# Performance work log

Hardware: AMD Instinct MI355X
Metric: run time of the kernel (lower is better)

The kernel has to match this reference:

```python
import jax, jax.numpy as jnp
import numpy as np

N, E, H, NH, S, EF, K = 25000, 400000, 64, 4, 16, 8, 2
HS = H // NH  # head size


def _ln(x, w, b):
    m = x.mean(-1, keepdims=True)
    v = ((x - m) ** 2).mean(-1, keepdims=True)
    return (x - m) / jnp.sqrt(v + 1e-5) * w + b


def _seg_softmax(scores, seg, n):
    # scores: [E, NH], seg: [E] -> softmax over edges sharing the same dest node
    mx = jax.ops.segment_max(scores, seg, num_segments=n)
    e = jnp.exp(scores - mx[seg])
    s = jax.ops.segment_sum(e, seg, num_segments=n)
    return e / (s[seg] + 1e-9)


def _edge_layer(h, x_s, src, dest, ef, w1, w2, proj, gated):
    # h: [N,H] (already layer-normed). Gather, fused per-edge MLP (no bias).
    inp = jnp.concatenate([h[src], h[dest], x_s[src], x_s[dest], ef], axis=-1)  # [E,168]
    raw = jnp.maximum(inp @ w1.T, 0.0) @ w2.T  # [E,NH]
    if gated:
        w = jax.nn.sigmoid(raw)
    else:
        w = _seg_softmax(jax.nn.leaky_relu(raw) / jnp.sqrt(jnp.asarray(HS, raw.dtype)), dest, N)
    msg = h.reshape(N, NH, HS)[src] * w[:, :, None]          # [E,NH,HS]
    agg = jax.ops.segment_sum(msg, dest, num_segments=N)     # [N,NH,HS]
    return agg.reshape(N, H) @ proj.T, w


def _mlp(x, w1, b1, w2, b2):
    return jnp.maximum(x @ w1.T + b1, 0.0) @ w2.T + b2


def _forward(x, x_s, edge_features, fwd_w1, fwd_w2, fwd_proj, rev_w1, rev_w2, rev_proj,
             ln_w, ln_b, r_w1, r_b1, r_w2, r_b2, z_w1, z_b1, z_w2, z_b2,
             c_w1, c_b1, c_w2, c_b2, edge_index):
    src, dest = edge_index[0], edge_index[1]
    # forward-direction stacked attention hops
    h_fwd, fwd_ws = x, []
    for k in range(K):
        h_norm = _ln(h_fwd, ln_w, ln_b)
        msg, w = _edge_layer(h_norm, x_s, src, dest, edge_features,
                             fwd_w1[k], fwd_w2[k], fwd_proj[k], gated=False)
        h_fwd = h_fwd + msg
        fwd_ws.append(w)
    fwd_ws = jnp.stack(fwd_ws, axis=-1)  # [E,NH,K]
    # reverse-direction stacked gating hops (edge direction flipped)
    h_rev, rev_ws = x, []
    for k in range(K):
        h_norm = _ln(h_rev, ln_w, ln_b)
        msg, w = _edge_layer(h_norm, x_s, dest, src, edge_features,
                             rev_w1[k], rev_w2[k], rev_proj[k], gated=True)
        h_rev = h_rev + msg
        rev_ws.append(w)
    rev_ws = jnp.stack(rev_ws, axis=-1)  # [E,NH,K]
    messages = jnp.concatenate([h_fwd - x, h_rev - x], axis=-1)  # [N,2H]
    gate_input = jnp.concatenate([x, messages], axis=-1)          # [N,3H]
    r_gate = jax.nn.sigmoid(_mlp(gate_input, r_w1, r_b1, r_w2, r_b2))
    z_gate = jax.nn.sigmoid(_mlp(gate_input, z_w1, z_b1, z_w2, z_b2))
    cand_in = jnp.concatenate([r_gate * x, messages], axis=-1)
    cand = jnp.tanh(_mlp(cand_in, c_w1, c_b1, c_w2, c_b2))
    final_h = (1.0 - z_gate) * x + z_gate * cand
    return final_h, fwd_ws, rev_ws, z_gate, r_gate


def setup_inputs() -> dict:
    key = jax.random.key(0)
    ks = jax.random.split(key, 20)
    mlp_in = 2 * H + 2 * S + EF  # 168
    width = 2 * H                # 128
    gi, gw = 3 * H, 3 * H        # 192, 192

    def nrm(k, shape, fan_in):
        return jax.random.normal(k, shape, jnp.float32) / np.sqrt(fan_in)

    return {
        'x': jax.random.normal(ks[0], (N, H), jnp.float32),
        'x_s': jax.random.normal(ks[1], (N, S), jnp.float32),
        'edge_index': jax.random.randint(ks[2], (2, E), 0, N, jnp.int32),
        'edge_features': jax.random.normal(ks[3], (E, EF), jnp.float32),
        'fwd_w1': nrm(ks[4], (K, width, mlp_in), mlp_in),
        'fwd_w2': nrm(ks[5], (K, NH, width), width),
        'fwd_proj': nrm(ks[6], (K, H, H), H),
        'rev_w1': nrm(ks[7], (K, width, mlp_in), mlp_in),
        'rev_w2': nrm(ks[8], (K, NH, width), width),
        'rev_proj': nrm(ks[9], (K, H, H), H),
        'ln_w': jnp.ones((H,), jnp.float32),
        'ln_b': jnp.zeros((H,), jnp.float32),
        'r_w1': nrm(ks[10], (gw, gi), gi), 'r_b1': jnp.zeros((gw,), jnp.float32),
        'r_w2': nrm(ks[11], (H, gw), gw), 'r_b2': jnp.zeros((H,), jnp.float32),
        'z_w1': nrm(ks[12], (gw, gi), gi), 'z_b1': jnp.zeros((gw,), jnp.float32),
        'z_w2': nrm(ks[13], (H, gw), gw), 'z_b2': jnp.zeros((H,), jnp.float32),
        'c_w1': nrm(ks[14], (gw, gi), gi), 'c_b1': jnp.zeros((gw,), jnp.float32),
        'c_w2': nrm(ks[15], (H, gw), gw), 'c_b2': jnp.zeros((H,), jnp.float32),
    }


def reference(x, x_s, edge_index, edge_features, fwd_w1, fwd_w2, fwd_proj,
              rev_w1, rev_w2, rev_proj, ln_w, ln_b, r_w1, r_b1, r_w2, r_b2,
              z_w1, z_b1, z_w2, z_b2, c_w1, c_b1, c_w2, c_b2):
    return _forward(x, x_s, edge_features, fwd_w1, fwd_w2, fwd_proj,
                    rev_w1, rev_w2, rev_proj, ln_w, ln_b,
                    r_w1, r_b1, r_w2, r_b2, z_w1, z_b1, z_w2, z_b2,
                    c_w1, c_b1, c_w2, c_b2, edge_index)
```

## Files before the change

### kernel.cpp

```cpp
#include <hip/hip_runtime.h>
#include <hip/hip_fp16.h>
#include <math.h>

#define NN 25000
#define EE 400000
#define HH 64
#define NHEAD 4
#define SDIM 16
#define EFDIM 8
#define KHOP 2
#define MIN 168
#define WID 128
#define GIN 192
#define KP 96

typedef __attribute__((ext_vector_type(8))) short bf16x8;
typedef __attribute__((ext_vector_type(4))) float f32x4;
typedef unsigned short ushortT;
typedef unsigned int uintT;

__device__ __forceinline__ float wave_sum64(float v) {
#pragma unroll
  for (int m = 1; m <= 32; m <<= 1) v += __shfl_xor(v, m, 64);
  return v;
}

__device__ __forceinline__ ushortT f2b(float f) {
  uintT u = __float_as_uint(f);
  return (ushortT)((u + 0x7FFFu + ((u >> 16) & 1u)) >> 16);
}
__device__ __forceinline__ float b2f(ushortT h) {
  return __uint_as_float(((uintT)h) << 16);
}

union U4H8 {
  uint4 u;
  __half2 h[4];
};

__device__ __forceinline__ __half2 relu2(__half2 v) {
  union { __half2 h; uintT u; } x;
  x.h = v;
  uintT mask = ((x.u & 0x80008000u) >> 15) * 0xFFFFu;
  x.u &= ~mask;
  return x.h;
}

__global__ void k_histo2(const int* __restrict__ src, const int* __restrict__ dst,
                         int* __restrict__ cnt_s, int* __restrict__ cnt_d) {
  int e = blockIdx.x * 256 + threadIdx.x;
  if (e < EE) {
    atomicAdd(&cnt_d[dst[e]], 1);
    atomicAdd(&cnt_s[src[e]], 1);
  }
}

__global__ void k_scan2(const int* __restrict__ cnt_d, const int* __restrict__ cnt_s,
                        int* __restrict__ rp_d, int* __restrict__ rp_s) {
  const int* cnt = blockIdx.x ? cnt_s : cnt_d;
  int* rp = blockIdx.x ? rp_s : rp_d;
  __shared__ int part[1024];
  int t = threadIdx.x;
  const int CH = (NN + 1023) / 1024;
  int base = t * CH;
  int s = 0;
  for (int i = 0; i < CH; ++i) {
    int j = base + i;
    if (j < NN) s += cnt[j];
  }
  part[t] = s;
  __syncthreads();
  for (int off = 1; off < 1024; off <<= 1) {
    int v = (t >= off) ? part[t - off] : 0;
    __syncthreads();
    part[t] += v;
    __syncthreads();
  }
  int run = (t == 0) ? 0 : part[t - 1];
  for (int i = 0; i < CH; ++i) {
    int j = base + i;
    if (j < NN) { rp[j] = run; run += cnt[j]; }
  }
  if (t == 1023) rp[NN] = run;
}

__global__ void k_scatter2(const int* __restrict__ src, const int* __restrict__ dst,
                           const int* __restrict__ rp_s, const int* __restrict__ rp_d,
                           int* __restrict__ cur_s, int* __restrict__ cur_d,
                           int* __restrict__ eid_s, int* __restrict__ eid_d) {
  int e = blockIdx.x * 256 + threadIdx.x;
  if (e < EE) {
    int nd = dst[e];
    int pd = atomicAdd(&cur_d[nd], 1);
    eid_d[rp_d[nd] + pd] = e;
    int ns = src[e];
    int ps = atomicAdd(&cur_s[ns], 1);
    eid_s[rp_s[ns] + ps] = e;
  }
}

__global__ __launch_bounds__(256) void k_sortseg2(const int* __restrict__ rp_d,
                                                  const int* __restrict__ rp_s,
                                                  int* __restrict__ eid_d,
                                                  int* __restrict__ eid_s) {
  int gw = blockIdx.x * 4 + (threadIdx.x >> 6);
  int lane = threadIdx.x & 63;
  if (gw >= 2 * NN) return;
  const int* rp = (gw < NN) ? rp_d : rp_s;
  int* eids = (gw < NN) ? eid_d : eid_s;
  int node = (gw < NN) ? gw : gw - NN;
  int beg = rp[node], end = rp[node + 1];
  int deg = end - beg;
  if (deg <= 1) return;
  if (deg <= 64) {
    int v = (lane < deg) ? eids[beg + lane] : 0x7fffffff;
#pragma unroll
    for (int k = 2; k <= 64; k <<= 1) {
#pragma unroll
      for (int j = k >> 1; j > 0; j >>= 1) {
        int other = __shfl_xor(v, j, 64);
        bool takeMin = (((lane & k) == 0) == ((lane & j) == 0));
        v = takeMin ? min(v, other) : max(v, other);
      }
    }
    if (lane < deg) eids[beg + lane] = v;
  } else if (lane == 0) {
    for (int i = beg + 1; i < end; ++i) {
      int v = eids[i];
      int j = i - 1;
      while (j >= beg && eids[j] > v) { eids[j + 1] = eids[j]; --j; }
      eids[j + 1] = v;
    }
  }
}

__global__ void k_mkpos2(const int* __restrict__ eid_d, const int* __restrict__ eid_s,
                         const int* __restrict__ src, const int* __restrict__ dst,
                         const float* __restrict__ ef, int4* __restrict__ pos_f,
                         int4* __restrict__ pos_r, uint4* __restrict__ efh_f,
                         uint4* __restrict__ efh_r) {
  int i = blockIdx.x * 256 + threadIdx.x;
  if (i >= EE) return;
  int e1 = eid_d[i];
  pos_f[i] = make_int4(e1, src[e1], dst[e1], 0);
  int e2 = eid_s[i];
  pos_r[i] = make_int4(e2, dst[e2], src[e2], 0);
  {
    float4 a0 = *(const float4*)(ef + (size_t)e1 * EFDIM);
    float4 a1 = *(const float4*)(ef + (size_t)e1 * EFDIM + 4);
    U4H8 u;
    u.h[0] = __floats2half2_rn(a0.x, a0.y);
    u.h[1] = __floats2half2_rn(a0.z, a0.w);
    u.h[2] = __floats2half2_rn(a1.x, a1.y);
    u.h[3] = __floats2half2_rn(a1.z, a1.w);
    efh_f[i] = u.u;
  }
  {
    float4 b0 = *(const float4*)(ef + (size_t)e2 * EFDIM);
    float4 b1 = *(const float4*)(ef + (size_t)e2 * EFDIM + 4);
    U4H8 u;
    u.h[0] = __floats2half2_rn(b0.x, b0.y);
    u.h[1] = __floats2half2_rn(b0.z, b0.w);
    u.h[2] = __floats2half2_rn(b1.x, b1.y);
    u.h[3] = __floats2half2_rn(b1.z, b1.w);
    efh_r[i] = u.u;
  }
}

#define PACKN (256 * KP + 512 + 256 + 4096)
__global__ void k_pack_bf(const float* __restrict__ fw1, const float* __restrict__ rw1,
                          const float* __restrict__ fw2, const float* __restrict__ rw2,
                          const float* __restrict__ fpj, const float* __restrict__ rpj,
                          ushortT* __restrict__ pAB_all, __half2* __restrict__ w1e2_all,
                          __half2* __restrict__ w22_all, ushortT* __restrict__ pj_all) {
  int y = blockIdx.y;
  const float* w1 = (y < 2) ? fw1 + (size_t)y * WID * MIN
                            : rw1 + (size_t)(y - 2) * WID * MIN;
  const float* w2 = (y < 2) ? fw2 + (size_t)y * NHEAD * WID
                            : rw2 + (size_t)(y - 2) * NHEAD * WID;
  const float* pj = (y < 2) ? fpj + (size_t)y * HH * HH
                            : rpj + (size_t)(y - 2) * HH * HH;
  int i = blockIdx.x * 256 + threadIdx.x;
  if (i < 256 * KP) {
    int j = i / KP, k = i % KP;
    float v = 0.f;
    if (k < 80) {
      int row = (j < 128) ? j : j - 128;
      int col = (j < 128) ? (k < 64 ? k : k + 64) : (k < 64 ? k + 64 : k + 80);
      v = w1[row * MIN + col];
    }
    pAB_all[(size_t)y * 256 * KP + i] = f2b(v);
  } else if (i < 256 * KP + 512) {
    int jj = i - 256 * KP;
    int f = jj >> 6, jp = jj & 63;
    w1e2_all[y * 512 + jj] =
        __floats2half2_rn(w1[(2 * jp) * MIN + 160 + f], w1[(2 * jp + 1) * MIN + 160 + f]);
  } else if (i < 256 * KP + 512 + 256) {
    int jj = i - 256 * KP - 512;
    int o = jj >> 6, jp = jj & 63;
    w22_all[y * 256 + jj] = __floats2half2_rn(w2[o * WID + 2 * jp], w2[o * WID + 2 * jp + 1]);
  } else if (i < PACKN) {
    int jj = i - 256 * KP - 512 - 256;
    pj_all[y * 4096 + jj] = f2b(pj[jj]);
  }
}

#define CW1 (GIN * GIN)
#define CW2 (HH * GIN)
__global__ void k_cvt6(const float* __restrict__ r_w1, const float* __restrict__ z_w1,
                       const float* __restrict__ c_w1, const float* __restrict__ r_w2,
                       const float* __restrict__ z_w2, const float* __restrict__ c_w2,
                       ushortT* __restrict__ rzw1, ushortT* __restrict__ cw1,
                       ushortT* __restrict__ rw2, ushortT* __restrict__ zw2,
                       ushortT* __restrict__ cw2) {
  int i = blockIdx.x * 256 + threadIdx.x;
  if (i < CW1) rzw1[i] = f2b(r_w1[i]);
  else if (i < 2 * CW1) rzw1[i] = f2b(z_w1[i - CW1]);
  else if (i < 3 * CW1) cw1[i - 2 * CW1] = f2b(c_w1[i - 2 * CW1]);
  else if (i < 3 * CW1 + CW2) rw2[i - 3 * CW1] = f2b(r_w2[i - 3 * CW1]);
  else if (i < 3 * CW1 + 2 * CW2) zw2[i - 3 * CW1 - CW2] = f2b(z_w2[i - 3 * CW1 - CW2]);
  else if (i < 3 * CW1 + 3 * CW2) cw2[i - 3 * CW1 - 2 * CW2] = f2b(c_w2[i - 3 * CW1 - 2 * CW2]);
}

__global__ __launch_bounds__(256) void k_ln_init(
    const float* __restrict__ x, const float* __restrict__ xs,
    const float* __restrict__ lw, const float* __restrict__ lb,
    ushortT* __restrict__ ncf0, ushortT* __restrict__ ncr0,
    ushortT* __restrict__ ncf1, ushortT* __restrict__ ncr1) {
  int t = threadIdx.x;
  int node = blockIdx.x * 4 + (t >> 6), lane = t & 63;
  if (node >= NN) return;
  float v = x[(size_t)node * HH + lane];
  float mean = wave_sum64(v) * (1.0f / 64.0f);
  float d = v - mean;
  float var = wave_sum64(d * d) * (1.0f / 64.0f);
  ushortT val = f2b(d * rsqrtf(var + 1e-5f) * lw[lane] + lb[lane]);
  ncf0[(size_t)node * KP + lane] = val;
  ncr0[(size_t)node * KP + lane] = val;
  if (lane < SDIM) {
    ushortT xv = f2b(xs[(size_t)node * SDIM + lane]);
    ncf0[(size_t)node * KP + HH + lane] = xv;
    ncr0[(size_t)node * KP + HH + lane] = xv;
    ncf1[(size_t)node * KP + HH + lane] = xv;
    ncr1[(size_t)node * KP + HH + lane] = xv;
    ncf0[(size_t)node * KP + 80 + lane] = 0;
    ncr0[(size_t)node * KP + 80 + lane] = 0;
    ncf1[(size_t)node * KP + 80 + lane] = 0;
    ncr1[(size_t)node * KP + 80 + lane] = 0;
  }
}

__global__ __launch_bounds__(256) void k_proj2(
    const ushortT* __restrict__ Af, const ushortT* __restrict__ Ar,
    const ushortT* __restrict__ Wf, const ushortT* __restrict__ Wr,
    ushortT* __restrict__ Cf, ushortT* __restrict__ Cr) {
  const ushortT* A = blockIdx.y ? Ar : Af;
  const ushortT* W = blockIdx.y ? Wr : Wf;
  ushortT* C = blockIdx.y ? Cr : Cf;
  int w = threadIdx.x >> 6, l = threadIdx.x & 63;
  int m0 = blockIdx.x * 64 + w * 16;
  int rowa = m0 + (l & 15);
  int kb = l >> 4;
  bf16x8 afr0 = {0,0,0,0,0,0,0,0}, afr1 = afr0, afr2 = afr0;
  if (rowa < NN) {
    const ushortT* ap = A + (size_t)rowa * KP + kb * 8;
    afr0 = *(const bf16x8*)(ap);
    afr1 = *(const bf16x8*)(ap + 32);
    afr2 = *(const bf16x8*)(ap + 64);
  }
  int crow = m0 + (l >> 4) * 4;
  int ccol0 = l & 15;
  for (int n0 = 0; n0 < 256; n0 += 64) {
    f32x4 acc[4];
#pragma unroll
    for (int n = 0; n < 4; ++n) acc[n] = (f32x4){0.f, 0.f, 0.f, 0.f};
    const ushortT* wbase = W + (size_t)(n0 + (l & 15)) * KP + kb * 8;
#pragma unroll
    for (int n = 0; n < 4; ++n) {
      const ushortT* wp = wbase + (size_t)(16 * n) * KP;
      acc[n] = __builtin_amdgcn_mfma_f32_16x16x32_bf16(afr0, *(const bf16x8*)(wp), acc[n], 0, 0, 0);
      acc[n] = __builtin_amdgcn_mfma_f32_16x16x32_bf16(afr1, *(const bf16x8*)(wp + 32), acc[n], 0, 0, 0);
      acc[n] = __builtin_amdgcn_mfma_f32_16x16x32_bf16(afr2, *(const bf16x8*)(wp + 64), acc[n], 0, 0, 0);
    }
#pragma unroll
    for (int n = 0; n < 4; ++n) {
      int col = n0 + ccol0 + n * 16;
#pragma unroll
      for (int r = 0; r < 4; ++r) {
        int row = crow + r;
        if (row < NN)
          C[(size_t)row * 256 + col] = __half_as_ushort(__float2half(acc[n][r]));
      }
    }
  }
}

template <int ACT, int BF16OUT, int KD>
__global__ __launch_bounds__(256) void k_gemm2(
    const ushortT* __restrict__ A, int lda, const ushortT* __restrict__ W,
    const float* __restrict__ bias, void* __restrict__ Cout, int ldc, int M, int Nc,
    const float* __restrict__ zv, const float* __restrict__ xp) {
  constexpr int KS = KD / 32;
  int w = threadIdx.x >> 6, l = threadIdx.x & 63;
  int m0 = blockIdx.x * 64 + w * 16;
  int rowa = m0 + (l & 15);
  int kb = l >> 4;
  bf16x8 afr[KS];
#pragma unroll
  for (int ks = 0; ks < KS; ++ks) {
    afr[ks] = (bf16x8){0, 0, 0, 0, 0, 0, 0, 0};
    if (rowa < M) afr[ks] = *(const bf16x8*)(A + (size_t)rowa * lda + ks * 32 + kb * 8);
  }
  int crow = m0 + (l >> 4) * 4;
  int ccol0 = l & 15;
  for (int n0 = 0; n0 < Nc; n0 += 64) {
    f32x4 acc[4];
#pragma unroll
    for (int n = 0; n < 4; ++n) acc[n] = (f32x4){0.f, 0.f, 0.f, 0.f};
    const ushortT* wbase = W + (size_t)(n0 + (l & 15)) * KD + kb * 8;
#pragma unroll
    for (int n = 0; n < 4; ++n) {
      const ushortT* wp = wbase + (size_t)(16 * n) * KD;
#pragma unroll
      for (int ks = 0; ks < KS; ++ks)
        acc[n] = __builtin_amdgcn_mfma_f32_16x16x32_bf16(afr[ks], *(const bf16x8*)(wp + ks * 32),
                                                         acc[n], 0, 0, 0);
    }
#pragma unroll
    for (int n = 0; n < 4; ++n) {
      int col = n0 + ccol0 + n * 16;
      float bv = bias ? bias[col] : 0.f;
#pragma unroll
      for (int r = 0; r < 4; ++r) {
        int row = crow + r;
        if (row < M) {
          float v = acc[n][r] + bv;
          if (ACT == 1) v = fmaxf(v, 0.f);
          else if (ACT == 2) v = 1.f / (1.f + expf(-v));
          else if (ACT == 3) v = tanhf(v);
          else if (ACT == 5) {
            float z = zv[(size_t)row * HH + col];
            float xv = xp[(size_t)row * HH + col];
            v = (1.f - z) * xv + z * tanhf(v);
          }
          if (BF16OUT)
            ((ushortT*)Cout)[(size_t)row * ldc + col] = f2b(v);
          else
            ((float*)Cout)[(size_t)row * ldc + col] = v;
        }
      }
    }
  }
}

__global__ __launch_bounds__(256) void k_gemm_rz(
    const ushortT* __restrict__ hid, const ushortT* __restrict__ rw2,
    const ushortT* __restrict__ zw2, const float* __restrict__ rb2,
    const float* __restrict__ zb2, float* __restrict__ outR, float* __restrict__ outZ,
    const float* __restrict__ x, ushortT* __restrict__ gi) {
  int y = blockIdx.y;
  const ushortT* A = hid + (y ? GIN : 0);
  const ushortT* W = y ? zw2 : rw2;
  const float* bias = y ? zb2 : rb2;
  float* C = y ? outZ : outR;
  constexpr int KS = GIN / 32;
  int w = threadIdx.x >> 6, l = threadIdx.x & 63;
  int m0 = blockIdx.x * 64 + w * 16;
  int rowa = m0 + (l & 15);
  int kb = l >> 4;
  bf16x8 afr[KS];
#pragma unroll
  for (int ks = 0; ks < KS; ++ks) {
    afr[ks] = (bf16x8){0, 0, 0, 0, 0, 0, 0, 0};
    if (rowa < NN) afr[ks] = *(const bf16x8*)(A + (size_t)rowa * 384 + ks * 32 + kb * 8);
  }
  int crow = m0 + (l >> 4) * 4;
  int ccol0 = l & 15;
  f32x4 acc[4];
#pragma unroll
  for (int n = 0; n < 4; ++n) acc[n] = (f32x4){0.f, 0.f, 0.f, 0.f};
  const ushortT* wbase = W + (size_t)(l & 15) * GIN + kb * 8;
#pragma unroll
  for (int n = 0; n < 4; ++n) {
    const ushortT* wp = wbase + (size_t)(16 * n) * GIN;
#pragma unroll
    for (int ks = 0; ks < KS; ++ks)
      acc[n] = __builtin_amdgcn_mfma_f32_16x16x32_bf16(afr[ks], *(const bf16x8*)(wp + ks * 32),
                                                       acc[n], 0, 0, 0);
  }
#pragma unroll
  for (int n = 0; n < 4; ++n) {
    int col = ccol0 + n * 16;
    float bv = bias[col];
#pragma unroll
    for (int r = 0; r < 4; ++r) {
      int row = crow + r;
      if (row < NN) {
        float v = acc[n][r] + bv;
        float sig = 1.f / (1.f + expf(-v));
        C[(size_t)row * HH + col] = sig;
        if (y == 0)
          gi[(size_t)row * GIN + col] = f2b(sig * x[(size_t)row * HH + col]);
      }
    }
  }
}

__global__ __launch_bounds__(256) void k_edge3(
    const ushortT* __restrict__ cABf, const ushortT* __restrict__ cABr,
    const int4* __restrict__ pos_f, const int4* __restrict__ pos_r,
    const uint4* __restrict__ efh_f, const uint4* __restrict__ efh_r,
    const __half2* __restrict__ w1e2_f, const __half2* __restrict__ w1e2_r,
    const __half2* __restrict__ w22_f, const __half2* __restrict__ w22_r,
    float* __restrict__ s_seq, float* __restrict__ outRW,
    float* __restrict__ ws_seq, int hop) {
  int y = blockIdx.y;
  const __half2* cAB2 = (const __half2*)(y ? cABr : cABf);
  const int4* pos = y ? pos_r : pos_f;
  const uint4* efh = y ? efh_r : efh_f;
  const __half2* w1e2 = y ? w1e2_r : w1e2_f;
  const __half2* w22 = y ? w22_r : w22_f;
  __shared__ __half2 w1e2_s[8][64];
  __shared__ __half2 w22_s[4][64];
  int t = threadIdx.x;
  for (int i = t; i < 512; i += 256) w1e2_s[i >> 6][i & 63] = w1e2[i];
  if (t < 256) w22_s[t >> 6][t & 63] = w22[t];
  __syncthreads();
  int es = t >> 2, q = t & 3;
  size_t ii = (size_t)blockIdx.x * 64 + es;
  int4 pr = pos[ii];
  const __half2* cA2 = cAB2 + (size_t)pr.y * 128;
  const __half2* cB2 = cAB2 + (size_t)pr.z * 128 + 64;
  U4H8 efu;
  efu.u = efh[ii];
  __half2 efb[8];
#pragma unroll
  for (int f2v = 0; f2v < 4; ++f2v) {
    efb[2 * f2v] = __half2half2(__low2half(efu.h[f2v]));
    efb[2 * f2v + 1] = __half2half2(__high2half(efu.h[f2v]));
  }
  float pf[4] = {0.f, 0.f, 0.f, 0.f};
#pragma unroll
  for (int c = 0; c < 4; ++c) {
    int jp0 = c * 16 + q * 4;
    U4H8 ua, ub;
    ua.u = *(const uint4*)(cA2 + jp0);
    ub.u = *(const uint4*)(cB2 + jp0);
    __half2 h2v[4];
#pragma unroll
    for (int i2 = 0; i2 < 4; ++i2) h2v[i2] = __hadd2(ua.h[i2], ub.h[i2]);
#pragma unroll
    for (int f = 0; f < 8; ++f) {
      U4H8 wv;
      wv.u = *(const uint4*)(&w1e2_s[f][jp0]);
#pragma unroll
      for (int i2 = 0; i2 < 4; ++i2) h2v[i2] = __hfma2(efb[f], wv.h[i2], h2v[i2]);
    }
#pragma unroll
    for (int i2 = 0; i2 < 4; ++i2) h2v[i2] = relu2(h2v[i2]);
#pragma unroll
    for (int o = 0; o < 4; ++o) {
      U4H8 wv;
      wv.u = *(const uint4*)(&w22_s[o][jp0]);
      __half2 p2 = __hmul2(h2v[0], wv.h[0]);
      p2 = __hfma2(h2v[1], wv.h[1], p2);
      p2 = __hfma2(h2v[2], wv.h[2], p2);
      p2 = __hfma2(h2v[3], wv.h[3], p2);
      pf[o] += __low2float(p2) + __high2float(p2);
    }
  }
#pragma unroll
  for (int m = 1; m <= 2; m <<= 1) {
    pf[0] += __shfl_xor(pf[0], m, 64);
    pf[1] += __shfl_xor(pf[1], m, 64);
    pf[2] += __shfl_xor(pf[2], m, 64);
    pf[3] += __shfl_xor(pf[3], m, 64);
  }
  float pv = (q == 0) ? pf[0] : (q == 1) ? pf[1] : (q == 2) ? pf[2] : pf[3];
  if (y) {
    float sig = 1.f / (1.f + expf(-pv));
    outRW[(size_t)pr.x * (NHEAD * KHOP) + q * KHOP + hop] = sig;
    ws_seq[ii * 4 + q] = sig;
  } else {
    s_seq[ii * 4 + q] = (pv > 0.f ? pv : 0.01f * pv) * 0.25f;
  }
}

__global__ __launch_bounds__(256) void k_softagg5(
    const ushortT* __restrict__ ncf, const ushortT* __restrict__ ncr,
    const float* __restrict__ s_seq, const float* __restrict__ ws_seq, int hop,
    const int* __restrict__ rp_d, const int* __restrict__ rp_s,
    const int4* __restrict__ pos_f, const int4* __restrict__ pos_r,
    ushortT* __restrict__ agg_f, ushortT* __restrict__ agg_r,
    float* __restrict__ wout) {
  int y = blockIdx.y;
  const ushortT* hn_bf = y ? ncr : ncf;
  const int* rp = y ? rp_s : rp_d;
  const int4* pos = y ? pos_r : pos_f;
  ushortT* agg = y ? agg_r : agg_f;
  __shared__ float w_s[4][64][4];
  __shared__ int ot_s[4][64];
  int t = threadIdx.x;
  int wvi = t >> 6, lane = t & 63;
  int node = blockIdx.x * 4 + wvi;
  if (node >= NN) return;
  int beg = rp[node], end = rp[node + 1];
  int deg = end - beg;
  bool small = (deg <= 64);
  float mxv = 0.f, invv = 0.f;
  int li = lane >> 2, o = lane & 3;
  if (deg > 0 && small) {
    int i0 = beg + li;
    if (y == 0) {
      int ee4[4];
      float sv[4];
#pragma unroll
      for (int u = 0; u < 4; ++u) {
        int idx = i0 + u * 16;
        bool val = idx < end;
        int4 pr = pos[val ? idx : beg];
        ee4[u] = pr.x;
        if (o == 0 && val) ot_s[wvi][li + u * 16] = pr.y * KP;
        float v = s_seq[(size_t)(val ? idx : beg) * 4 + o];
        sv[u] = val ? v : -1e30f;
      }
      float mx = fmaxf(fmaxf(sv[0], sv[1]), fmaxf(sv[2], sv[3]));
#pragma unroll
      for (int m = 4; m <= 32; m <<= 1) mx = fmaxf(mx, __shfl_xor(mx, m, 64));
      float ex[4];
      float sum = 0.f;
#pragma unroll
      for (int u = 0; u < 4; ++u) {
        ex[u] = (sv[u] > -1e29f) ? expf(sv[u] - mx) : 0.f;
        sum += ex[u];
      }
#pragma unroll
      for (int m = 4; m <= 32; m <<= 1) sum += __shfl_xor(sum, m, 64);
      float inv = 1.f / (sum + 1e-9f);
#pragma unroll
      for (int u = 0; u < 4; ++u) {
        if (i0 + u * 16 < end) {
          float wv = ex[u] * inv;
          wout[(size_t)ee4[u] * (NHEAD * KHOP) + o * KHOP + hop] = wv;
          w_s[wvi][li + u * 16][o] = wv;
        }
      }
    } else {
#pragma unroll
      for (int u = 0; u < 4; ++u) {
        int idx = i0 + u * 16;
        bool val = idx < end;
        if (val) {
          if (o == 0) {
            int4 pr = pos[idx];
            ot_s[wvi][li + u * 16] = pr.y * KP;
          }
          w_s[wvi][li + u * 16][o] = ws_seq[(size_t)idx * 4 + o];
        }
      }
    }
  } else if (deg > 0) {
    if (y == 0) {
      float mx = -1e30f;
      for (int ii = beg + li; ii < end; ii += 16)
        mx = fmaxf(mx, s_seq[(size_t)ii * 4 + o]);
#pragma unroll
      for (int m = 4; m <= 32; m <<= 1) mx = fmaxf(mx, __shfl_xor(mx, m, 64));
      float sum = 0.f;
      for (int ii = beg + li; ii < end; ii += 16)
        sum += expf(s_seq[(size_t)ii * 4 + o] - mx);
#pragma unroll
      for (int m = 4; m <= 32; m <<= 1) sum += __shfl_xor(sum, m, 64);
      float inv = 1.f / (sum + 1e-9f);
      for (int ii = beg + li; ii < end; ii += 16) {
        wout[(size_t)pos[ii].x * (NHEAD * KHOP) + o * KHOP + hop] =
            expf(s_seq[(size_t)ii * 4 + o] - mx) * inv;
      }
      mxv = mx;
      invv = inv;
    }
  }
  int hd = lane >> 4;
  float acc = 0.f;
  if (small) {
    for (int ii = 0; ii < deg; ii += 8) {
#pragma unroll
      for (int u = 0; u < 8; ++u) {
        int ed = ii + u;
        int edc = (ed < deg) ? ed : 0;
        int ot = ot_s[wvi][edc];
        float w = w_s[wvi][edc][hd];
        float hv = b2f(hn_bf[(size_t)ot + lane]);
        acc += ((ed < deg) ? w : 0.f) * hv;
      }
    }
  } else {
    float mx_hd = 0.f, inv_hd = 0.f;
    if (y == 0) {
      mx_hd = __shfl(mxv, hd, 64);
      inv_hd = __shfl(invv, hd, 64);
    }
    for (int ii = beg; ii < end; ++ii) {
      int4 pr = pos[ii];
      float w;
      if (y == 0)
        w = expf(s_seq[(size_t)ii * 4 + hd] - mx_hd) * inv_hd;
      else
        w = ws_seq[(size_t)ii * 4 + hd];
      acc += w * b2f(hn_bf[(size_t)pr.y * KP + lane]);
    }
  }
  agg[(size_t)node * HH + lane] = f2b(acc);
}

template <int DO_LN, int DO_GATE>
__global__ __launch_bounds__(256) void k_projout(
    const ushortT* __restrict__ agg_f, const ushortT* __restrict__ agg_r,
    const ushortT* __restrict__ pj_f, const ushortT* __restrict__ pj_r,
    float* __restrict__ h_f, float* __restrict__ h_r,
    ushortT* __restrict__ ncf_n, ushortT* __restrict__ ncr_n,
    const float* __restrict__ lnw, const float* __restrict__ lnb,
    const float* __restrict__ x, ushortT* __restrict__ gi) {
  int y = blockIdx.y;
  const ushortT* A = y ? agg_r : agg_f;
  const ushortT* W = y ? pj_r : pj_f;
  float* h = y ? h_r : h_f;
  ushortT* ncat_n = y ? ncr_n : ncf_n;
  int w = threadIdx.x >> 6, l = threadIdx.x & 63;
  int m0 = blockIdx.x * 64 + w * 16;
  int rowa = m0 + (l & 15);
  int kb = l >> 4;
  bf16x8 afr0 = {0, 0, 0, 0, 0, 0, 0, 0}, afr1 = afr0;
  if (rowa < NN) {
    afr0 = *(const bf16x8*)(A + (size_t)rowa * HH + kb * 8);
    afr1 = *(const bf16x8*)(A + (size_t)rowa * HH + 32 + kb * 8);
  }
  f32x4 acc[4];
#pragma unroll
  for (int n = 0; n < 4; ++n) acc[n] = (f32x4){0.f, 0.f, 0.f, 0.f};
  const ushortT* wbase = W + (size_t)(l & 15) * HH + kb * 8;
#pragma unroll
  for (int n = 0; n < 4; ++n) {
    const ushortT* wp = wbase + (size_t)(16 * n) * HH;
    acc[n] = __builtin_amdgcn_mfma_f32_16x16x32_bf16(afr0, *(const bf16x8*)(wp), acc[n], 0, 0, 0);
    acc[n] = __builtin_amdgcn_mfma_f32_16x16x32_bf16(afr1, *(const bf16x8*)(wp + 32), acc[n], 0, 0, 0);
  }
  int crow = m0 + (l >> 4) * 4;
  int ccol0 = l & 15;
#pragma unroll
  for (int r = 0; r < 4; ++r) {
    int row = crow + r;
    if (row >= NN) continue;
    float hv[4];
#pragma unroll
    for (int n = 0; n < 4; ++n)
      hv[n] = h[(size_t)row * HH + ccol0 + n * 16] + acc[n][r];
    float s = hv[0] + hv[1] + hv[2] + hv[3];
#pragma unroll
    for (int m = 1; m <= 8; m <<= 1) s += __shfl_xor(s, m, 64);
    float mean = s * (1.0f / 64.0f);
    float ss = 0.f;
#pragma unroll
    for (int n = 0; n < 4; ++n) {
      float d = hv[n] - mean;
      ss += d * d;
    }
#pragma unroll
    for (int m = 1; m <= 8; m <<= 1) ss += __shfl_xor(ss, m, 64);
    float rstd = rsqrtf(ss * (1.0f / 64.0f) + 1e-5f);
#pragma unroll
    for (int n = 0; n < 4; ++n) {
      int col = ccol0 + n * 16;
      size_t g = (size_t)row * HH + col;
      h[g] = hv[n];
      if (DO_LN)
        ncat_n[(size_t)row * KP + col] = f2b((hv[n] - mean) * rstd * lnw[col] + lnb[col]);
      if (DO_GATE) {
        float xv = x[g];
        if (y == 0) {
          gi[(size_t)row * GIN + col] = f2b(xv);
          gi[(size_t)row * GIN + 64 + col] = f2b(hv[n] - xv);
        } else {
          gi[(size_t)row * GIN + 128 + col] = f2b(hv[n] - xv);
        }
      }
    }
  }
}

extern "C" void kernel_launch(void* const* d_in, const int* in_sizes, int n_in,
                              void* d_out, int out_size, void* d_ws, size_t ws_size,
                              hipStream_t stream) {
  const float* x = (const float*)d_in[0];
  const float* xs = (const float*)d_in[1];
  const int* ei = (const int*)d_in[2];
  const float* ef = (const float*)d_in[3];
  const float* fw1 = (const float*)d_in[4];
  const float* fw2 = (const float*)d_in[5];
  const float* fpj = (const float*)d_in[6];
  const float* rw1 = (const float*)d_in[7];
  const float* rw2 = (const float*)d_in[8];
  const float* rpj = (const float*)d_in[9];
  const float* lnw = (const float*)d_in[10];
  const float* lnb = (const float*)d_in[11];
  const float* r_w1 = (const float*)d_in[12];
  const float* r_b1 = (const float*)d_in[13];
  const float* r_w2 = (const float*)d_in[14];
  const float* r_b2 = (const float*)d_in[15];
  const float* z_w1 = (const float*)d_in[16];
  const float* z_b1 = (const float*)d_in[17];
  const float* z_w2 = (const float*)d_in[18];
  const float* z_b2 = (const float*)d_in[19];
  const float* c_w1 = (const float*)d_in[20];
  const float* c_b1 = (const float*)d_in[21];
  const float* c_w2 = (const float*)d_in[22];
  const float* c_b2 = (const float*)d_in[23];
  const int* srcp = ei;
  const int* dstp = ei + EE;

  float* outF = (float*)d_out;
  float* outFW = outF + (size_t)NN * HH;
  float* outRW = outFW + (size_t)EE * NHEAD * KHOP;
  float* outZ = outRW + (size_t)EE * NHEAD * KHOP;
  float* outR = outZ + (size_t)NN * HH;

  char* Wb = (char*)d_ws;
  size_t off = 0;
  auto alloc = [&](size_t bytes) -> void* {
    void* p = Wb + off;
    off += (bytes + 255) & ~(size_t)255;
    return p;
  };
  float* h_fwd = (float*)alloc((size_t)NN * HH * 4);
  float* h_rev = (float*)alloc((size_t)NN * HH * 4);
  ushortT* ncat_f0 = (ushortT*)alloc((size_t)NN * KP * 2);
  ushortT* ncat_r0 = (ushortT*)alloc((size_t)NN * KP * 2);
  ushortT* ncat_f1 = (ushortT*)alloc((size_t)NN * KP * 2);
  ushortT* ncat_r1 = (ushortT*)alloc((size_t)NN * KP * 2);
  float* s_seq = (float*)alloc((size_t)EE * NHEAD * 4);
  float* ws_seq = (float*)alloc((size_t)EE * NHEAD * 4);
  char* big = (char*)alloc((size_t)2 * NN * 256 * 2);
  ushortT* cAB_f = (ushortT*)big;
  ushortT* cAB_r = (ushortT*)(big + (size_t)NN * 256 * 2);
  ushortT* hid_bf = (ushortT*)big;
  ushortT* gi_bf = (ushortT*)alloc((size_t)NN * GIN * 2);
  ushortT* agg_f = (ushortT*)alloc((size_t)NN * HH * 2);
  ushortT* agg_r = (ushortT*)alloc((size_t)NN * HH * 2);
  ushortT* packAB_bf = (ushortT*)alloc((size_t)4 * 256 * KP * 2);
  __half2* w1e2h = (__half2*)alloc((size_t)4 * 512 * 4);
  __half2* w22h = (__half2*)alloc((size_t)4 * 256 * 4);
  ushortT* pj_bf = (ushortT*)alloc((size_t)4 * 4096 * 2);
  ushortT* rzw1_bf = (ushortT*)alloc((size_t)384 * GIN * 2);
  ushortT* rw2_bf = (ushortT*)alloc((size_t)HH * GIN * 2);
  ushortT* zw2_bf = (ushortT*)alloc((size_t)HH * GIN * 2);
  ushortT* cw1_bf = (ushortT*)alloc((size_t)GIN * GIN * 2);
  ushortT* cw2_bf = (ushortT*)alloc((size_t)HH * GIN * 2);
  float* rz_b1 = (float*)alloc(384 * 4);
  int* rp_d = (int*)alloc((NN + 8) * 4);
  int* rp_s = (int*)alloc((NN + 8) * 4);
  int* cur2 = (int*)alloc((size_t)2 * NN * 4);
  int* cur_d = cur2;
  int* cur_s = cur2 + NN;
  int* eid_d = (int*)alloc((size_t)EE * 4);
  int* eid_s = (int*)alloc((size_t)EE * 4);
  int4* pos_f = (int4*)alloc((size_t)EE * 16);
  int4* pos_r = (int4*)alloc((size_t)EE * 16);
  uint4* efh_f = (uint4*)alloc((size_t)EE * 16);
  uint4* efh_r = (uint4*)alloc((size_t)EE * 16);

  (void)hipMemcpyAsync(h_fwd, x, (size_t)NN * HH * 4, hipMemcpyDeviceToDevice, stream);
  (void)hipMemcpyAsync(h_rev, x, (size_t)NN * HH * 4, hipMemcpyDeviceToDevice, stream);
  (void)hipMemcpyAsync(rz_b1, r_b1, GIN * 4, hipMemcpyDeviceToDevice, stream);
  (void)hipMemcpyAsync(rz_b1 + GIN, z_b1, GIN * 4, hipMemcpyDeviceToDevice, stream);

  const int EB = (EE + 255) / 256, NW = (NN + 3) / 4;
  const int PB = (PACKN + 255) / 256;

  dim3 gPack(PB, 4);
  k_pack_bf<<<gPack, 256, 0, stream>>>(fw1, rw1, fw2, rw2, fpj, rpj, packAB_bf,
                                       w1e2h, w22h, pj_bf);
  k_cvt6<<<(3 * CW1 + 3 * CW2 + 255) / 256, 256, 0, stream>>>(
      r_w1, z_w1, c_w1, r_w2, z_w2, c_w2, rzw1_bf, cw1_bf, rw2_bf, zw2_bf, cw2_bf);

  (void)hipMemsetAsync(cur2, 0, (size_t)2 * NN * 4, stream);
  k_histo2<<<EB, 256, 0, stream>>>(srcp, dstp, cur_s, cur_d);
  k_scan2<<<2, 1024, 0, stream>>>(cur_d, cur_s, rp_d, rp_s);
  (void)hipMemsetAsync(cur2, 0, (size_t)2 * NN * 4, stream);
  k_scatter2<<<EB, 256, 0, stream>>>(srcp, dstp, rp_s, rp_d, cur_s, cur_d, eid_s, eid_d);
  k_sortseg2<<<(2 * NN + 3) / 4, 256, 0, stream>>>(rp_d, rp_s, eid_d, eid_s);
  k_mkpos2<<<EB, 256, 0, stream>>>(eid_d, eid_s, srcp, dstp, ef, pos_f, pos_r, efh_f, efh_r);

  k_ln_init<<<NW, 256, 0, stream>>>(x, xs, lnw, lnb, ncat_f0, ncat_r0, ncat_f1, ncat_r1);

  const int MB64 = (NN + 63) / 64;
  dim3 gProj(MB64, 2), gEdge(EE / 64, 2), gAgg(NW, 2), gPO(MB64, 2);
  for (int k = 0; k < KHOP; ++k) {
    const ushortT* nf = k ? ncat_f1 : ncat_f0;
    const ushortT* nr = k ? ncat_r1 : ncat_r0;
    k_proj2<<<gProj, 256, 0, stream>>>(nf, nr,
                                       packAB_bf + (size_t)k * 256 * KP,
                                       packAB_bf + (size_t)(2 + k) * 256 * KP,
                                       cAB_f, cAB_r);
    k_edge3<<<gEdge, 256, 0, stream>>>(cAB_f, cAB_r, pos_f, pos_r, efh_f, efh_r,
                                       w1e2h + (size_t)k * 512,
                                       w1e2h + (size_t)(2 + k) * 512,
                                       w22h + (size_t)k * 256,
                                       w22h + (size_t)(2 + k) * 256,
                                       s_seq, outRW, ws_seq, k);
    k_softagg5<<<gAgg, 256, 0, stream>>>(nf, nr, s_seq, ws_seq, k, rp_d, rp_s,
                                         pos_f, pos_r, agg_f, agg_r, outFW);
    if (k == 0)
      k_projout<1, 0><<<gPO, 256, 0, stream>>>(
          agg_f, agg_r, pj_bf + (size_t)k * 4096, pj_bf + (size_t)(2 + k) * 4096,
          h_fwd, h_rev, ncat_f1, ncat_r1, lnw, lnb, x, gi_bf);
    else
      k_projout<0, 1><<<gPO, 256, 0, stream>>>(
          agg_f, agg_r, pj_bf + (size_t)k * 4096, pj_bf + (size_t)(2 + k) * 4096,
          h_fwd, h_rev, ncat_f1, ncat_r1, lnw, lnb, x, gi_bf);
  }

  k_gemm2<1, 1, GIN><<<MB64, 256, 0, stream>>>(gi_bf, GIN, rzw1_bf, rz_b1, hid_bf,
                                               384, NN, 384, nullptr, nullptr);
  dim3 gRZ(MB64, 2);
  k_gemm_rz<<<gRZ, 256, 0, stream>>>(hid_bf, rw2_bf, zw2_bf, r_b2, z_b2, outR, outZ,
                                     x, gi_bf);
  k_gemm2<1, 1, GIN><<<MB64, 256, 0, stream>>>(gi_bf, GIN, cw1_bf, c_b1, hid_bf, GIN,
                                               NN, GIN, nullptr, nullptr);
  k_gemm2<5, 0, GIN><<<MB64, 256, 0, stream>>>(hid_bf, GIN, cw2_bf, c_b2, outF, HH,
                                               NN, HH, outZ, x);
}
```

Before: 517.6 us.

## Split node GEMMs across column tiles and shrink blocks to one wave

Result: faster. 498.6 us (median of 2 runs) (-3.7%).

```diff
diff --git a/kernel.cpp b/kernel.cpp
--- a/kernel.cpp
+++ b/kernel.cpp
@@ -254,9 +254,11 @@
     const ushortT* __restrict__ Af, const ushortT* __restrict__ Ar,
     const ushortT* __restrict__ Wf, const ushortT* __restrict__ Wr,
     ushortT* __restrict__ Cf, ushortT* __restrict__ Cr) {
-  const ushortT* A = blockIdx.y ? Ar : Af;
-  const ushortT* W = blockIdx.y ? Wr : Wf;
-  ushortT* C = blockIdx.y ? Cr : Cf;
+  int dir = blockIdx.y & 1;
+  int n0 = (blockIdx.y >> 1) * 64;
+  const ushortT* A = dir ? Ar : Af;
+  const ushortT* W = dir ? Wr : Wf;
+  ushortT* C = dir ? Cr : Cf;
   int w = threadIdx.x >> 6, l = threadIdx.x & 63;
   int m0 = blockIdx.x * 64 + w * 16;
   int rowa = m0 + (l & 15);
@@ -270,39 +272,38 @@
   }
   int crow = m0 + (l >> 4) * 4;
   int ccol0 = l & 15;
-  for (int n0 = 0; n0 < 256; n0 += 64) {
-    f32x4 acc[4];
-#pragma unroll
-    for (int n = 0; n < 4; ++n) acc[n] = (f32x4){0.f, 0.f, 0.f, 0.f};
-    const ushortT* wbase = W + (size_t)(n0 + (l & 15)) * KP + kb * 8;
-#pragma unroll
-    for (int n = 0; n < 4; ++n) {
-      const ushortT* wp = wbase + (size_t)(16 * n) * KP;
-      acc[n] = __builtin_amdgcn_mfma_f32_16x16x32_bf16(afr0, *(const bf16x8*)(wp), acc[n], 0, 0, 0);
-      acc[n] = __builtin_amdgcn_mfma_f32_16x16x32_bf16(afr1, *(const bf16x8*)(wp + 32), acc[n], 0, 0, 0);
-      acc[n] = __builtin_amdgcn_mfma_f32_16x16x32_bf16(afr2, *(const bf16x8*)(wp + 64), acc[n], 0, 0, 0);
-    }
-#pragma unroll
-    for (int n = 0; n < 4; ++n) {
-      int col = n0 + ccol0 + n * 16;
-#pragma unroll
-      for (int r = 0; r < 4; ++r) {
-        int row = crow + r;
-        if (row < NN)
-          C[(size_t)row * 256 + col] = __half_as_ushort(__float2half(acc[n][r]));
-      }
+  f32x4 acc[4];
+#pragma unroll
+  for (int n = 0; n < 4; ++n) acc[n] = (f32x4){0.f, 0.f, 0.f, 0.f};
+  const ushortT* wbase = W + (size_t)(n0 + (l & 15)) * KP + kb * 8;
+#pragma unroll
+  for (int n = 0; n < 4; ++n) {
+    const ushortT* wp = wbase + (size_t)(16 * n) * KP;
+    acc[n] = __builtin_amdgcn_mfma_f32_16x16x32_bf16(afr0, *(const bf16x8*)(wp), acc[n], 0, 0, 0);
+    acc[n] = __builtin_amdgcn_mfma_f32_16x16x32_bf16(afr1, *(const bf16x8*)(wp + 32), acc[n], 0, 0, 0);
+    acc[n] = __builtin_amdgcn_mfma_f32_16x16x32_bf16(afr2, *(const bf16x8*)(wp + 64), acc[n], 0, 0, 0);
+  }
+#pragma unroll
+  for (int n = 0; n < 4; ++n) {
+    int col = n0 + ccol0 + n * 16;
+#pragma unroll
+    for (int r = 0; r < 4; ++r) {
+      int row = crow + r;
+      if (row < NN)
+        C[(size_t)row * 256 + col] = __half_as_ushort(__float2half(acc[n][r]));
     }
   }
 }
 
 template <int ACT, int BF16OUT, int KD>
-__global__ __launch_bounds__(256) void k_gemm2(
+__global__ __launch_bounds__(64) void k_gemm3(
     const ushortT* __restrict__ A, int lda, const ushortT* __restrict__ W,
-    const float* __restrict__ bias, void* __restrict__ Cout, int ldc, int M, int Nc,
+    const float* __restrict__ bias, void* __restrict__ Cout, int ldc, int M,
     const float* __restrict__ zv, const float* __restrict__ xp) {
   constexpr int KS = KD / 32;
-  int w = threadIdx.x >> 6, l = threadIdx.x & 63;
-  int m0 = blockIdx.x * 64 + w * 16;
+  int l = threadIdx.x;
+  int m0 = blockIdx.x * 16;
+  int n0 = blockIdx.y * 64;
   int rowa = m0 + (l & 15);
   int kb = l >> 4;
   bf16x8 afr[KS];
@@ -311,49 +312,47 @@
     afr[ks] = (bf16x8){0, 0, 0, 0, 0, 0, 0, 0};
     if (rowa < M) afr[ks] = *(const bf16x8*)(A + (size_t)rowa * lda + ks * 32 + kb * 8);
   }
+  f32x4 acc[4];
+#pragma unroll
+  for (int n = 0; n < 4; ++n) acc[n] = (f32x4){0.f, 0.f, 0.f, 0.f};
+  const ushortT* wbase = W + (size_t)(n0 + (l & 15)) * KD + kb * 8;
+#pragma unroll
+  for (int n = 0; n < 4; ++n) {
+    const ushortT* wp = wbase + (size_t)(16 * n) * KD;
+#pragma unroll
+    for (int ks = 0; ks < KS; ++ks)
+      acc[n] = __builtin_amdgcn_mfma_f32_16x16x32_bf16(afr[ks], *(const bf16x8*)(wp + ks * 32),
+                                                       acc[n], 0, 0, 0);
+  }
   int crow = m0 + (l >> 4) * 4;
-  int ccol0 = l & 15;
-  for (int n0 = 0; n0 < Nc; n0 += 64) {
-    f32x4 acc[4];
-#pragma unroll
-    for (int n = 0; n < 4; ++n) acc[n] = (f32x4){0.f, 0.f, 0.f, 0.f};
-    const ushortT* wbase = W + (size_t)(n0 + (l & 15)) * KD + kb * 8;
-#pragma unroll
-    for (int n = 0; n < 4; ++n) {
-      const ushortT* wp = wbase + (size_t)(16 * n) * KD;
-#pragma unroll
-      for (int ks = 0; ks < KS; ++ks)
-        acc[n] = __builtin_amdgcn_mfma_f32_16x16x32_bf16(afr[ks], *(const bf16x8*)(wp + ks * 32),
-                                                         acc[n], 0, 0, 0);
-    }
-#pragma unroll
-    for (int n = 0; n < 4; ++n) {
-      int col = n0 + ccol0 + n * 16;
-      float bv = bias ? bias[col] : 0.f;
-#pragma unroll
-      for (int r = 0; r < 4; ++r) {
-        int row = crow + r;
-        if (row < M) {
-          float v = acc[n][r] + bv;
-          if (ACT == 1) v = fmaxf(v, 0.f);
-          else if (ACT == 2) v = 1.f / (1.f + expf(-v));
-          else if (ACT == 3) v = tanhf(v);
-          else if (ACT == 5) {
-            float z = zv[(size_t)row * HH + col];
-            float xv = xp[(size_t)row * HH + col];
-            v = (1.f - z) * xv + z * tanhf(v);
-          }
-          if (BF16OUT)
-            ((ushortT*)Cout)[(size_t)row * ldc + col] = f2b(v);
-          else
-            ((float*)Cout)[(size_t)row * ldc + col] = v;
+  int ccol0 = n0 + (l & 15);
+#pragma unroll
+  for (int n = 0; n < 4; ++n) {
+    int col = ccol0 + n * 16;
+    float bv = bias ? bias[col] : 0.f;
+#pragma unroll
+    for (int r = 0; r < 4; ++r) {
+      int row = crow + r;
+      if (row < M) {
+        float v = acc[n][r] + bv;
+        if (ACT == 1) v = fmaxf(v, 0.f);
+        else if (ACT == 2) v = 1.f / (1.f + expf(-v));
+        else if (ACT == 3) v = tanhf(v);
+        else if (ACT == 5) {
+          float z = zv[(size_t)row * HH + col];
+          float xv = xp[(size_t)row * HH + col];
+          v = (1.f - z) * xv + z * tanhf(v);
         }
-      }
-    }
-  }
-}
-
-__global__ __launch_bounds__(256) void k_gemm_rz(
+        if (BF16OUT)
+          ((ushortT*)Cout)[(size_t)row * ldc + col] = f2b(v);
+        else
+          ((float*)Cout)[(size_t)row * ldc + col] = v;
+      }
+    }
+  }
+}
+
+__global__ __launch_bounds__(64) void k_gemm_rz3(
     const ushortT* __restrict__ hid, const ushortT* __restrict__ rw2,
     const ushortT* __restrict__ zw2, const float* __restrict__ rb2,
     const float* __restrict__ zb2, float* __restrict__ outR, float* __restrict__ outZ,
@@ -364,8 +363,8 @@
   const float* bias = y ? zb2 : rb2;
   float* C = y ? outZ : outR;
   constexpr int KS = GIN / 32;
-  int w = threadIdx.x >> 6, l = threadIdx.x & 63;
-  int m0 = blockIdx.x * 64 + w * 16;
+  int l = threadIdx.x;
+  int m0 = blockIdx.x * 16;
   int rowa = m0 + (l & 15);
   int kb = l >> 4;
   bf16x8 afr[KS];
@@ -374,8 +373,6 @@
     afr[ks] = (bf16x8){0, 0, 0, 0, 0, 0, 0, 0};
     if (rowa < NN) afr[ks] = *(const bf16x8*)(A + (size_t)rowa * 384 + ks * 32 + kb * 8);
   }
-  int crow = m0 + (l >> 4) * 4;
-  int ccol0 = l & 15;
   f32x4 acc[4];
 #pragma unroll
   for (int n = 0; n < 4; ++n) acc[n] = (f32x4){0.f, 0.f, 0.f, 0.f};
@@ -388,6 +385,8 @@
       acc[n] = __builtin_amdgcn_mfma_f32_16x16x32_bf16(afr[ks], *(const bf16x8*)(wp + ks * 32),
                                                        acc[n], 0, 0, 0);
   }
+  int crow = m0 + (l >> 4) * 4;
+  int ccol0 = l & 15;
 #pragma unroll
   for (int n = 0; n < 4; ++n) {
     int col = ccol0 + n * 16;
@@ -614,7 +613,7 @@
 }
 
 template <int DO_LN, int DO_GATE>
-__global__ __launch_bounds__(256) void k_projout(
+__global__ __launch_bounds__(64) void k_projout(
     const ushortT* __restrict__ agg_f, const ushortT* __restrict__ agg_r,
     const ushortT* __restrict__ pj_f, const ushortT* __restrict__ pj_r,
     float* __restrict__ h_f, float* __restrict__ h_r,
@@ -626,8 +625,8 @@
   const ushortT* W = y ? pj_r : pj_f;
   float* h = y ? h_r : h_f;
   ushortT* ncat_n = y ? ncr_n : ncf_n;
-  int w = threadIdx.x >> 6, l = threadIdx.x & 63;
-  int m0 = blockIdx.x * 64 + w * 16;
+  int l = threadIdx.x;
+  int m0 = blockIdx.x * 16;
   int rowa = m0 + (l & 15);
   int kb = l >> 4;
   bf16x8 afr0 = {0, 0, 0, 0, 0, 0, 0, 0}, afr1 = afr0;
@@ -793,7 +792,8 @@
   k_ln_init<<<NW, 256, 0, stream>>>(x, xs, lnw, lnb, ncat_f0, ncat_r0, ncat_f1, ncat_r1);
 
   const int MB64 = (NN + 63) / 64;
-  dim3 gProj(MB64, 2), gEdge(EE / 64, 2), gAgg(NW, 2), gPO(MB64, 2);
+  const int MB16 = (NN + 15) / 16;
+  dim3 gProj(MB64, 8), gEdge(EE / 64, 2), gAgg(NW, 2), gPO(MB16, 2);
   for (int k = 0; k < KHOP; ++k) {
     const ushortT* nf = k ? ncat_f1 : ncat_f0;
     const ushortT* nr = k ? ncat_r1 : ncat_r0;
@@ -810,22 +810,22 @@
     k_softagg5<<<gAgg, 256, 0, stream>>>(nf, nr, s_seq, ws_seq, k, rp_d, rp_s,
                                          pos_f, pos_r, agg_f, agg_r, outFW);
     if (k == 0)
-      k_projout<1, 0><<<gPO, 256, 0, stream>>>(
+      k_projout<1, 0><<<gPO, 64, 0, stream>>>(
           agg_f, agg_r, pj_bf + (size_t)k * 4096, pj_bf + (size_t)(2 + k) * 4096,
           h_fwd, h_rev, ncat_f1, ncat_r1, lnw, lnb, x, gi_bf);
     else
-      k_projout<0, 1><<<gPO, 256, 0, stream>>>(
+      k_projout<0, 1><<<gPO, 64, 0, stream>>>(
           agg_f, agg_r, pj_bf + (size_t)k * 4096, pj_bf + (size_t)(2 + k) * 4096,
           h_fwd, h_rev, ncat_f1, ncat_r1, lnw, lnb, x, gi_bf);
   }
 
-  k_gemm2<1, 1, GIN><<<MB64, 256, 0, stream>>>(gi_bf, GIN, rzw1_bf, rz_b1, hid_bf,
-                                               384, NN, 384, nullptr, nullptr);
-  dim3 gRZ(MB64, 2);
-  k_gemm_rz<<<gRZ, 256, 0, stream>>>(hid_bf, rw2_bf, zw2_bf, r_b2, z_b2, outR, outZ,
-                                     x, gi_bf);
-  k_gemm2<1, 1, GIN><<<MB64, 256, 0, stream>>>(gi_bf, GIN, cw1_bf, c_b1, hid_bf, GIN,
-                                               NN, GIN, nullptr, nullptr);
-  k_gemm2<5, 0, GIN><<<MB64, 256, 0, stream>>>(hid_bf, GIN, cw2_bf, c_b2, outF, HH,
-                                               NN, HH, outZ, x);
-}
+  dim3 gRZ1(MB16, 6), gRZ2(MB16, 2), gC1(MB16, 3), gF(MB16, 1);
+  k_gemm3<1, 1, GIN><<<gRZ1, 64, 0, stream>>>(gi_bf, GIN, rzw1_bf, rz_b1, hid_bf,
+                                              384, NN, nullptr, nullptr);
+  k_gemm_rz3<<<gRZ2, 64, 0, stream>>>(hid_bf, rw2_bf, zw2_bf, r_b2, z_b2, outR, outZ,
+                                      x, gi_bf);
+  k_gemm3<1, 1, GIN><<<gC1, 64, 0, stream>>>(gi_bf, GIN, cw1_bf, c_b1, hid_bf, GIN,
+                                             NN, nullptr, nullptr);
+  k_gemm3<5, 0, GIN><<<gF, 64, 0, stream>>>(hid_bf, GIN, cw2_bf, c_b2, outF, HH, NN,
+                                            outZ, x);
+}
```
